# Optimization experiments

Measured on AMD Instinct MI355X. Metric: run time of the kernel, lower is better.

Reference implementation:

```python
import math
import jax, jax.numpy as jnp
import numpy as np

H = 4  # num heads
D = 512
MLP = 1024
EPS = 1e-6


def _ln(x, g, b):
    m = x.mean(-1, keepdims=True)
    v = ((x - m) ** 2).mean(-1, keepdims=True)
    return (x - m) / jnp.sqrt(v + EPS) * g + b


def _heads(x):
    B, S, d = x.shape
    return x.reshape(B, S, H, d // H).transpose(0, 2, 1, 3)  # [B,H,S,hd]


def _att(q, k, v, Wo, bo):
    # q,k,v: [B,S,D] already projected
    hd = q.shape[-1] // H
    qh, kh, vh = _heads(q), _heads(k), _heads(v)
    scores = jnp.einsum('bhqd,bhkd->bhqk', qh, kh) / math.sqrt(hd)
    probs = jax.nn.softmax(scores, axis=-1)
    ctx = jnp.einsum('bhqk,bhkd->bhqd', probs, vh)
    B, _, S, _ = ctx.shape
    ctx = ctx.transpose(0, 2, 1, 3).reshape(B, S, H * hd)
    return ctx @ Wo + bo


def setup_inputs() -> dict:
    key = jax.random.key(0)
    ks = jax.random.split(key, 32)
    i = iter(range(32))
    def w(shape, scale=0.02):
        return jax.random.normal(ks[next(i)], shape, dtype=jnp.float32) * scale
    inp = {
        'x1': jax.random.normal(ks[next(i)], (16, 1024, D), dtype=jnp.float32),
        'x2': jax.random.normal(ks[next(i)], (16, 1024, D), dtype=jnp.float32),
        'ln1_g': jnp.ones((D,), jnp.float32), 'ln1_b': jnp.zeros((D,), jnp.float32),
        'ln2_g': jnp.ones((D,), jnp.float32), 'ln2_b': jnp.zeros((D,), jnp.float32),
        'lnf_g': jnp.ones((D,), jnp.float32), 'lnf_b': jnp.zeros((D,), jnp.float32),
    }
    for name in ['q1', 'k1', 'v1', 'q2', 'k2', 'v2', 'q12', 'k12', 'v12', 'o']:
        inp['W' + name] = w((D, D))
        inp['b' + name] = jnp.zeros((D,), jnp.float32)
    inp['W1'] = w((D, MLP)); inp['b1'] = jnp.zeros((MLP,), jnp.float32)
    inp['W2'] = w((MLP, D)); inp['b2'] = jnp.zeros((D,), jnp.float32)
    return inp


def reference(x1, x2, ln1_g, ln1_b, ln2_g, ln2_b, lnf_g, lnf_b,
              Wq1, bq1, Wk1, bk1, Wv1, bv1,
              Wq2, bq2, Wk2, bk2, Wv2, bv2,
              Wq12, bq12, Wk12, bk12, Wv12, bv12,
              Wo, bo, W1, b1, W2, b2):
    identity = x1
    x1n = _ln(x1, ln1_g, ln1_b)
    x2n = _ln(x2, ln2_g, ln2_b)
    # stream-1 self-attention with residual onto normalized input
    src1 = x1n + _att(x1n @ Wq1 + bq1, x1n @ Wk1 + bk1, x1n @ Wv1 + bv1, Wo, bo)
    # stream-2 self-attention
    src2 = x2n + _att(x2n @ Wq2 + bq2, x2n @ Wk2 + bk2, x2n @ Wv2 + bv2, Wo, bo)
    # cross attention: query from src1, key/value from src2
    attn_out = _att(src1 @ Wq12 + bq12, src2 @ Wk12 + bk12, src2 @ Wv12 + bv12, Wo, bo)
    x = attn_out + identity
    h = _ln(x, lnf_g, lnf_b)
    h = jax.nn.gelu(h @ W1 + b1, approximate=False) @ W2 + b2
    return x + h
```

## Files before the change

kernel.cpp:

```cpp
#include <hip/hip_runtime.h>
#include <math.h>


#define SEQ   1024
#define DM    512
#define HDIM  128
#define MTOK  16384
#define MLPD  1024
#define SC2   ((float)(0.08838834764831845 * 1.4426950408889634))

typedef short bf16x8 __attribute__((ext_vector_type(8)));
typedef float f32x4  __attribute__((ext_vector_type(4)));
typedef float f32x16 __attribute__((ext_vector_type(16)));
typedef unsigned short us4 __attribute__((ext_vector_type(4)));

typedef unsigned int u32g __attribute__((address_space(1)));
typedef unsigned int u32l __attribute__((address_space(3)));

static __device__ __forceinline__ unsigned short f2b(float f) {
  union { float f; unsigned u; } v; v.f = f;
  unsigned r = v.u + 0x7FFFu + ((v.u >> 16) & 1u);
  return (unsigned short)(r >> 16);
}
static __device__ __forceinline__ float b2f(unsigned short h) {
  union { unsigned u; float f; } v; v.u = ((unsigned)h) << 16;
  return v.f;
}
static __device__ __forceinline__ unsigned pk2t(float a, float b) {
  union { float f; unsigned u; } va, vb; va.f = a; vb.f = b;
  return __builtin_amdgcn_perm(vb.u, va.u, 0x07060302u);
}
static __device__ __forceinline__ float ex2(float x) {
  float r; asm("v_exp_f32 %0, %1" : "=v"(r) : "v"(x)); return r;
}
static __device__ __forceinline__ void gl_lds16(const void* g, void* l) {
  __builtin_amdgcn_global_load_lds((u32g*)g, (u32l*)l, 16, 0, 0);
}

struct P12 { const float* p[12]; };
struct P9  { const float* p[9]; };

__global__ __launch_bounds__(256) void prep_kernel(P12 ws, P9 bs,
                                                   unsigned short* __restrict__ WT0,
                                                   unsigned short* __restrict__ W1t,
                                                   unsigned short* __restrict__ W2t,
                                                   float* __restrict__ bcc) {
  int bid = blockIdx.x;
  if (bid >= 3584) {
    int i = (bid - 3584) * 256 + threadIdx.x;
    if (i < 4608) bcc[i] = bs.p[i >> 9][i & 511];
    return;
  }
  __shared__ float t[32][33];
  const float* W; unsigned short* Wt; int K, N, tt;
  if (bid < 2560)      { int wi = bid >> 8; W = ws.p[wi]; Wt = WT0 + (size_t)wi * 262144; K = 512; N = 512; tt = bid & 255; }
  else if (bid < 3072) { W = ws.p[10]; Wt = W1t; K = 512;  N = 1024; tt = bid - 2560; }
  else                 { W = ws.p[11]; Wt = W2t; K = 1024; N = 512;  tt = bid - 3072; }
  int ntiles = N >> 5;
  int bx = tt % ntiles, by = tt / ntiles;
  int n0 = bx * 32, k0 = by * 32;
  int tx = threadIdx.x & 31, ty = threadIdx.x >> 5;
#pragma unroll
  for (int i = 0; i < 32; i += 8)
    t[ty + i][tx] = W[(size_t)(k0 + ty + i) * N + n0 + tx];
  __syncthreads();
#pragma unroll
  for (int i = 0; i < 32; i += 8)
    Wt[(size_t)(n0 + ty + i) * K + k0 + tx] = f2b(t[tx][ty + i]);
}

__global__ __launch_bounds__(256) void ln_kernel(const float* __restrict__ X0,
                                                 const float* __restrict__ X1,
                                                 const float* __restrict__ g0w,
                                                 const float* __restrict__ b0w,
                                                 const float* __restrict__ g1w,
                                                 const float* __restrict__ b1w,
                                                 unsigned short* __restrict__ out0,
                                                 unsigned short* __restrict__ out1) {
  int idx  = blockIdx.x * 4 + (threadIdx.x >> 6);
  int sel  = idx >> 14;
  int row  = idx & 16383;
  const float* X = sel ? X1 : X0;
  const float* gw = sel ? g1w : g0w;
  const float* bw = sel ? b1w : b0w;
  unsigned short* outB = sel ? out1 : out0;
  int lane = threadIdx.x & 63;
  const float4* xr = (const float4*)(X + (size_t)row * DM);
  float4 a = xr[lane];
  float4 c = xr[lane + 64];
  float s  = a.x + a.y + a.z + a.w + c.x + c.y + c.z + c.w;
  float s2 = a.x*a.x + a.y*a.y + a.z*a.z + a.w*a.w
           + c.x*c.x + c.y*c.y + c.z*c.z + c.w*c.w;
#pragma unroll
  for (int off = 1; off < 64; off <<= 1) {
    s  += __shfl_xor(s,  off, 64);
    s2 += __shfl_xor(s2, off, 64);
  }
  float mean = s * (1.0f / 512.0f);
  float var  = s2 * (1.0f / 512.0f) - mean * mean;
  float rstd = rsqrtf(var + 1e-6f);
  const float4* gv = (const float4*)gw;
  const float4* bv = (const float4*)bw;
  float4 g1 = gv[lane], g2 = gv[lane + 64];
  float4 b1 = bv[lane], b2 = bv[lane + 64];
  us4 o1, o2;
  o1.x = f2b((a.x - mean) * rstd * g1.x + b1.x);
  o1.y = f2b((a.y - mean) * rstd * g1.y + b1.y);
  o1.z = f2b((a.z - mean) * rstd * g1.z + b1.z);
  o1.w = f2b((a.w - mean) * rstd * g1.w + b1.w);
  o2.x = f2b((c.x - mean) * rstd * g2.x + b2.x);
  o2.y = f2b((c.y - mean) * rstd * g2.y + b2.y);
  o2.z = f2b((c.z - mean) * rstd * g2.z + b2.z);
  o2.w = f2b((c.w - mean) * rstd * g2.w + b2.w);
  *(us4*)(outB + (size_t)row * DM + lane * 4)        = o1;
  *(us4*)(outB + (size_t)row * DM + (lane + 64) * 4) = o2;
}

template <int RES, bool GELU_ACT, int OMODE>
__global__ __launch_bounds__(256, 2) void gemm_kernel(const unsigned short* __restrict__ A,
                                                      const unsigned short* __restrict__ A1,
                                                      const unsigned short* __restrict__ Bt,
                                                      const float* __restrict__ bias,
                                                      const void* __restrict__ res,
                                                      float* __restrict__ outF,
                                                      unsigned short* __restrict__ outB,
                                                      unsigned short* __restrict__ outV,
                                                      int M, int N, int K) {
  int nT = N >> 7;
  int mT = M >> 7;
  int xcd = blockIdx.x & 7;
  int idx = blockIdx.x >> 3;
  int mPerX = mT >> 3;
  int q = idx / nT;
  int tm = xcd * mPerX + q;
  int tn = idx - q * nT;
  int m0 = tm << 7, n0 = tn << 7;
  int tid = threadIdx.x, lane = tid & 63, w = tid >> 6;
  int m16 = lane & 15, q4 = lane >> 4;
  int wr = (w & 1) << 6, wc = (w >> 1) << 6;
  __shared__ unsigned short Alds[2][128 * 64];
  __shared__ unsigned short Blds[2][128 * 64];
  f32x4 acc[4][4] = {};

  const unsigned short* Aeff = A;
  const unsigned short* Bteff = Bt;
  const float* biaseff = bias;
  if (OMODE == 3) {
    int half = tm >> 7;
    Bteff = Bt + (size_t)half * 3 * 262144;
    biaseff = bias + half * 1536;
  }
  if (OMODE == 4) {
    if (tn >= 4) Aeff = A1;
  }

  int srow = lane >> 3;
  int scol = ((lane & 7) ^ srow) << 3;
  const unsigned short* Ag = Aeff  + (size_t)(m0 + w * 8 + srow) * K + scol;
  const unsigned short* Bg = Bteff + (size_t)(n0 + w * 8 + srow) * K + scol;
  int ldst = w * 512;

#pragma unroll
  for (int it = 0; it < 4; ++it) {
    gl_lds16(Ag + (size_t)it * 32 * K, Alds[0] + it * 2048 + ldst);
    gl_lds16(Bg + (size_t)it * 32 * K, Blds[0] + it * 2048 + ldst);
  }

  int nk = K >> 6;
  for (int ks = 0; ks < nk; ++ks) {
    int cur = ks & 1, nxt = cur ^ 1;
    __syncthreads();
    if (ks + 1 < nk) {
      int k0n = (ks + 1) << 6;
#pragma unroll
      for (int it = 0; it < 4; ++it) {
        gl_lds16(Ag + (size_t)it * 32 * K + k0n, Alds[nxt] + it * 2048 + ldst);
        gl_lds16(Bg + (size_t)it * 32 * K + k0n, Blds[nxt] + it * 2048 + ldst);
      }
    }
    const unsigned short* Ar = Alds[cur];
    const unsigned short* Br = Blds[cur];
#pragma unroll
    for (int kk = 0; kk < 64; kk += 32) {
      bf16x8 af[4], bfr[4];
#pragma unroll
      for (int i = 0; i < 4; ++i) {
        int row = wr + i * 16 + m16;
        af[i] = *(const bf16x8*)(Ar + row * 64 + ((((kk >> 3) + q4) ^ (m16 & 7)) << 3));
      }
#pragma unroll
      for (int j = 0; j < 4; ++j) {
        int row = wc + j * 16 + m16;
        bfr[j] = *(const bf16x8*)(Br + row * 64 + ((((kk >> 3) + q4) ^ (m16 & 7)) << 3));
      }
#pragma unroll
      for (int i = 0; i < 4; ++i)
#pragma unroll
        for (int j = 0; j < 4; ++j)
          acc[i][j] = __builtin_amdgcn_mfma_f32_16x16x32_bf16(af[i], bfr[j], acc[i][j], 0, 0, 0);
    }
  }
  if (OMODE == 3 || OMODE == 4) {
    if (n0 < 1024) {
      int stride = (OMODE == 3) ? 1024 : 512;
      unsigned short* ob = outB;
      int coff = 0;
      if (OMODE == 4 && n0 >= 512) { ob = outB + (size_t)MTOK * 512; coff = 512; }
      float sc = (n0 < 512) ? SC2 : 1.0f;
#pragma unroll
      for (int i = 0; i < 4; ++i) {
#pragma unroll
        for (int r = 0; r < 4; ++r) {
          int row = m0 + wr + i * 16 + q4 * 4 + r;
#pragma unroll
          for (int j = 0; j < 4; ++j) {
            int col = n0 + wc + j * 16 + m16;
            ob[(size_t)row * stride + col - coff] = f2b((acc[i][j][r] + biaseff[col]) * sc);
          }
        }
      }
    } else {
#pragma unroll
      for (int i = 0; i < 4; ++i) {
        int row0 = m0 + wr + i * 16 + q4 * 4;
        int s = row0 & 1023, bl = row0 >> 10;
        s = (s & ~12) | ((s & 4) << 1) | ((s & 8) >> 1);
#pragma unroll
        for (int j = 0; j < 4; ++j) {
          int col = n0 + wc + j * 16 + m16;
          int hh = (col - 1024) >> 7, hd = col & 127;
          float bb = biaseff[col];
          us4 pkv;
          pkv.x = f2b(acc[i][j][0] + bb);
          pkv.y = f2b(acc[i][j][1] + bb);
          pkv.z = f2b(acc[i][j][2] + bb);
          pkv.w = f2b(acc[i][j][3] + bb);
          *(us4*)(outV + (((size_t)(bl * 4 + hh)) * HDIM + hd) * SEQ + s) = pkv;
        }
      }
    }
  } else {
#pragma unroll
    for (int i = 0; i < 4; ++i) {
#pragma unroll
      for (int r = 0; r < 4; ++r) {
        int row = m0 + wr + i * 16 + q4 * 4 + r;
#pragma unroll
        for (int j = 0; j < 4; ++j) {
          int col = n0 + wc + j * 16 + m16;
          float v = acc[i][j][r] + bias[col];
          if (RES == 1) v += ((const float*)res)[(size_t)row * N + col];
          if (RES == 2) v += b2f(((const unsigned short*)res)[(size_t)row * N + col]);
          if (GELU_ACT) v = 0.5f * v * (1.0f + erff(v * 0.70710678118654752f));
          if (OMODE == 1) outF[(size_t)row * N + col] = v;
          else            outB[(size_t)row * N + col] = f2b(v);
        }
      }
    }
  }
}

__global__ __launch_bounds__(256, 2) void attn_kernel(const unsigned short* __restrict__ Qb_,
                                                      const unsigned short* __restrict__ Kb_,
                                                      int tstride,
                                                      const unsigned short* __restrict__ Vt,
                                                      unsigned short* __restrict__ CTX,
                                                      int pairs_per_xcd) {
  int xcd = blockIdx.x & 7;
  int i   = blockIdx.x >> 3;
  int pair = xcd * pairs_per_xcd + (i >> 3);
  int qt   = i & 7;
  int b = pair >> 2, h = pair & 3;
  int tid = threadIdx.x, lane = tid & 63, w = tid >> 6;
  int m32 = lane & 31, hf = lane >> 5;
  size_t qkoff = ((size_t)b * SEQ) * tstride + h * HDIM;
  const unsigned short* Qg = Qb_ + qkoff;
  const unsigned short* Kg = Kb_ + qkoff;
  const unsigned short* Vp = Vt + (size_t)pair * HDIM * SEQ;

  __shared__ unsigned short Klds[2][64 * 128];
  __shared__ unsigned short Vlds[2][128 * 64];

  int qrow0 = qt * 128 + w * 32;
  bf16x8 qf[8];
  {
    const unsigned short* qp = Qg + (size_t)(qrow0 + m32) * tstride + hf * 8;
#pragma unroll
    for (int ks = 0; ks < 8; ++ks) qf[ks] = *(const bf16x8*)(qp + ks * 16);
  }
  bf16x8 onesf;
#pragma unroll
  for (int j = 0; j < 8; ++j) onesf[j] = (short)0x3F80;

  const unsigned short* kp0 = Kg + (size_t)(16 * w + (lane >> 4)) * tstride
                              + (((lane & 15) ^ (lane >> 4)) << 3);
  const unsigned short* kp1 = Kg + (size_t)(16 * w + 4 + (lane >> 4)) * tstride
                              + (((lane & 15) ^ ((lane >> 4) + 4)) << 3);
  const unsigned short* vp0 = Vp + (size_t)(32 * w + (lane >> 3)) * SEQ
                              + (((lane & 7) ^ (lane >> 3)) << 3);
  int klo = 16 * w * 128;
  int vlo = 32 * w * 64;

  gl_lds16(kp0,               Klds[0] + klo);
  gl_lds16(kp1,               Klds[0] + klo + 4 * 128);
  gl_lds16(kp0 + 8 * tstride, Klds[0] + klo + 8 * 128);
  gl_lds16(kp1 + 8 * tstride, Klds[0] + klo + 12 * 128);
  gl_lds16(vp0,               Vlds[0] + vlo);
  gl_lds16(vp0 + 8 * SEQ,     Vlds[0] + vlo + 8 * 64);
  gl_lds16(vp0 + 16 * SEQ,    Vlds[0] + vlo + 16 * 64);
  gl_lds16(vp0 + 24 * SEQ,    Vlds[0] + vlo + 24 * 64);

  f32x16 o0 = {}, o1 = {}, o2 = {}, o3 = {};
  f32x16 lacc = {};

  for (int kt = 0; kt < 16; ++kt) {
    int cur = kt & 1, nxt = cur ^ 1;
    __syncthreads();
    if (kt < 15) {
      kp0 += 64 * tstride; kp1 += 64 * tstride; vp0 += 64;
      gl_lds16(kp0,               Klds[nxt] + klo);
      gl_lds16(kp1,               Klds[nxt] + klo + 4 * 128);
      gl_lds16(kp0 + 8 * tstride, Klds[nxt] + klo + 8 * 128);
      gl_lds16(kp1 + 8 * tstride, Klds[nxt] + klo + 12 * 128);
      gl_lds16(vp0,               Vlds[nxt] + vlo);
      gl_lds16(vp0 + 8 * SEQ,     Vlds[nxt] + vlo + 8 * 64);
      gl_lds16(vp0 + 16 * SEQ,    Vlds[nxt] + vlo + 16 * 64);
      gl_lds16(vp0 + 24 * SEQ,    Vlds[nxt] + vlo + 24 * 64);
    }
    const unsigned short* Kr = Klds[cur];
    const unsigned short* Vr = Vlds[cur];

    f32x16 sc0 = {}, sc1 = {};
#pragma unroll
    for (int ks = 0; ks < 8; ++ks) {
      int ch = 2 * ks + hf;
      bf16x8 kf0 = *(const bf16x8*)(Kr + m32 * 128 + ((ch ^ (m32 & 7)) << 3));
      sc0 = __builtin_amdgcn_mfma_f32_32x32x16_bf16(kf0, qf[ks], sc0, 0, 0, 0);
      int k1r = 32 + m32;
      bf16x8 kf1 = *(const bf16x8*)(Kr + k1r * 128 + ((ch ^ (k1r & 7)) << 3));
      sc1 = __builtin_amdgcn_mfma_f32_32x32x16_bf16(kf1, qf[ks], sc1, 0, 0, 0);
    }

    bf16x8 pa[4];
#pragma unroll
    for (int t = 0; t < 2; ++t) {
      const f32x16& sc = t ? sc1 : sc0;
#pragma unroll
      for (int g = 0; g < 2; ++g) {
        union { unsigned u[4]; bf16x8 v; } uu;
        uu.u[0] = pk2t(ex2(sc[8*g+0]), ex2(sc[8*g+1]));
        uu.u[1] = pk2t(ex2(sc[8*g+2]), ex2(sc[8*g+3]));
        uu.u[2] = pk2t(ex2(sc[8*g+4]), ex2(sc[8*g+5]));
        uu.u[3] = pk2t(ex2(sc[8*g+6]), ex2(sc[8*g+7]));
        pa[2*t + g] = uu.v;
      }
    }

#pragma unroll
    for (int ks = 0; ks < 4; ++ks) {
      int ch = 2 * ks + hf;
      int sw = m32 & 7;
      lacc = __builtin_amdgcn_mfma_f32_32x32x16_bf16(pa[ks], onesf, lacc, 0, 0, 0);
      {
        bf16x8 vf = *(const bf16x8*)(Vr + m32 * 64 + ((ch ^ sw) << 3));
        o0 = __builtin_amdgcn_mfma_f32_32x32x16_bf16(pa[ks], vf, o0, 0, 0, 0);
      }
      {
        bf16x8 vf = *(const bf16x8*)(Vr + (32 + m32) * 64 + ((ch ^ sw) << 3));
        o1 = __builtin_amdgcn_mfma_f32_32x32x16_bf16(pa[ks], vf, o1, 0, 0, 0);
      }
      {
        bf16x8 vf = *(const bf16x8*)(Vr + (64 + m32) * 64 + ((ch ^ sw) << 3));
        o2 = __builtin_amdgcn_mfma_f32_32x32x16_bf16(pa[ks], vf, o2, 0, 0, 0);
      }
      {
        bf16x8 vf = *(const bf16x8*)(Vr + (96 + m32) * 64 + ((ch ^ sw) << 3));
        o3 = __builtin_amdgcn_mfma_f32_32x32x16_bf16(pa[ks], vf, o3, 0, 0, 0);
      }
    }
  }

  size_t obase = ((size_t)b * SEQ + qrow0) * DM + h * HDIM;
#pragma unroll
  for (int g = 0; g < 4; ++g) {
#pragma unroll
    for (int r = 0; r < 4; ++r) {
      int reg = 4 * g + r;
      int rowl = 8 * g + 4 * hf + r;
      float inv = 1.0f / lacc[reg];
      size_t off = obase + (size_t)rowl * DM + m32;
      CTX[off]      = f2b(o0[reg] * inv);
      CTX[off + 32] = f2b(o1[reg] * inv);
      CTX[off + 64] = f2b(o2[reg] * inv);
      CTX[off + 96] = f2b(o3[reg] * inv);
    }
  }
}

extern "C" void kernel_launch(void* const* d_in, const int* in_sizes, int n_in,
                              void* d_out, int out_size, void* d_ws, size_t ws_size,
                              hipStream_t stream) {
  const float* x1    = (const float*)d_in[0];
  const float* x2    = (const float*)d_in[1];
  const float* ln1_g = (const float*)d_in[2];
  const float* ln1_b = (const float*)d_in[3];
  const float* ln2_g = (const float*)d_in[4];
  const float* ln2_b = (const float*)d_in[5];
  const float* lnf_g = (const float*)d_in[6];
  const float* lnf_b = (const float*)d_in[7];
  P12 wsrc;
  for (int i = 0; i < 10; ++i) wsrc.p[i] = (const float*)d_in[8 + 2 * i];
  wsrc.p[10] = (const float*)d_in[28];
  wsrc.p[11] = (const float*)d_in[30];
  P9 bsrc;
  for (int i = 0; i < 9; ++i) bsrc.p[i] = (const float*)d_in[9 + 2 * i];
  const float* bo   = (const float*)d_in[27];
  const float* b1   = (const float*)d_in[29];
  const float* b2   = (const float*)d_in[31];

  char* ws = (char*)d_ws;
  size_t off = 0;
  auto alloc = [&](size_t bytes) -> char* {
    char* p = ws + off;
    off += (bytes + 255) & ~(size_t)255;
    return p;
  };
  unsigned short* WT0 = (unsigned short*)alloc((size_t)10 * 512 * 512 * 2);
  auto WT = [&](int i) { return WT0 + (size_t)i * 262144; };
  unsigned short* W1t = (unsigned short*)alloc((size_t)1024 * 512 * 2);
  unsigned short* W2t = (unsigned short*)alloc((size_t)512 * 1024 * 2);
  float*          bcc = (float*)alloc(4608 * 4);
  unsigned short* XN  = (unsigned short*)alloc((size_t)2 * MTOK * DM * 2);
  unsigned short* QKb = (unsigned short*)alloc((size_t)2 * MTOK * 1024 * 2);
  unsigned short* Vtb = (unsigned short*)alloc((size_t)128 * HDIM * SEQ * 2);
  unsigned short* CT  = (unsigned short*)alloc((size_t)2 * MTOK * DM * 2);
  float*          Xf  = (float*)alloc((size_t)MTOK * DM * 4);
  unsigned short* XN1 = XN + (size_t)MTOK * DM;
  unsigned short* MID = QKb;
  unsigned short* HN  = Vtb;
  float* bias_self  = bcc;
  float* bias_cross = bcc + 3072;

  prep_kernel<<<3602, 256, 0, stream>>>(wsrc, bsrc, WT0, W1t, W2t, bcc);

  ln_kernel<<<2 * MTOK / 4, 256, 0, stream>>>(x1, x2, ln1_g, ln1_b, ln2_g, ln2_b, XN, XN1);

  gemm_kernel<0, false, 3><<<3072, 256, 0, stream>>>(XN, nullptr, WT0, bias_self,
      nullptr, nullptr, QKb, Vtb, 32768, 1536, 512);

  attn_kernel<<<128 * 8, 256, 0, stream>>>(QKb, QKb + 512, 1024, Vtb, CT, 16);

  gemm_kernel<2, false, 0><<<1024, 256, 0, stream>>>(CT, nullptr, WT(9), bo, XN,
      nullptr, XN, nullptr, 32768, 512, 512);

  gemm_kernel<0, false, 4><<<1536, 256, 0, stream>>>(XN, XN1, WT(6), bias_cross,
      nullptr, nullptr, QKb, Vtb, 16384, 1536, 512);

  attn_kernel<<<64 * 8, 256, 0, stream>>>(QKb, QKb + (size_t)MTOK * 512, 512, Vtb, CT, 8);

  gemm_kernel<1, false, 1><<<512, 256, 0, stream>>>(CT, nullptr, WT(9), bo, x1,
      Xf, nullptr, nullptr, 16384, 512, 512);

  ln_kernel<<<MTOK / 4, 256, 0, stream>>>(Xf, Xf, lnf_g, lnf_b, lnf_g, lnf_b, HN, HN);

  gemm_kernel<0, true,  0><<<1024, 256, 0, stream>>>(HN, nullptr, W1t, b1,
      nullptr, nullptr, MID, nullptr, 16384, 1024, 512);
  gemm_kernel<1, false, 1><<<512, 256, 0, stream>>>(MID, nullptr, W2t, b2,
      Xf, (float*)d_out, nullptr, nullptr, 16384, 512, 1024);
}
```

Before: 515.1 us.

## Software-pipeline attention loop so QK of next tile overlaps PV of current

Restructures the flash-attention inner loop into a software pipeline: the QK^T MFMAs for tile t+1 are issued alongside the PV MFMAs for tile t, with the exp/pack step deferred. The goal is to hide the exp2/packing latency and the LDS reads behind independent matrix work. The cost is an extra barrier per iteration, because the buffer being restaged must be fully consumed first, and more live registers for the second set of probability fragments, which could lower occupancy.

```diff
diff --git a/kernel.cpp b/kernel.cpp
--- a/kernel.cpp
+++ b/kernel.cpp
@@ -301,84 +301,103 @@
   int klo = 16 * w * 128;
   int vlo = 32 * w * 64;
 
-  gl_lds16(kp0,               Klds[0] + klo);
-  gl_lds16(kp1,               Klds[0] + klo + 4 * 128);
-  gl_lds16(kp0 + 8 * tstride, Klds[0] + klo + 8 * 128);
-  gl_lds16(kp1 + 8 * tstride, Klds[0] + klo + 12 * 128);
-  gl_lds16(vp0,               Vlds[0] + vlo);
-  gl_lds16(vp0 + 8 * SEQ,     Vlds[0] + vlo + 8 * 64);
-  gl_lds16(vp0 + 16 * SEQ,    Vlds[0] + vlo + 16 * 64);
-  gl_lds16(vp0 + 24 * SEQ,    Vlds[0] + vlo + 24 * 64);
+  auto stage = [&](unsigned short* Kb, unsigned short* Vb) {
+    gl_lds16(kp0,               Kb + klo);
+    gl_lds16(kp1,               Kb + klo + 4 * 128);
+    gl_lds16(kp0 + 8 * tstride, Kb + klo + 8 * 128);
+    gl_lds16(kp1 + 8 * tstride, Kb + klo + 12 * 128);
+    gl_lds16(vp0,               Vb + vlo);
+    gl_lds16(vp0 + 8 * SEQ,     Vb + vlo + 8 * 64);
+    gl_lds16(vp0 + 16 * SEQ,    Vb + vlo + 16 * 64);
+    gl_lds16(vp0 + 24 * SEQ,    Vb + vlo + 24 * 64);
+  };
+  auto adv = [&]() { kp0 += 64 * tstride; kp1 += 64 * tstride; vp0 += 64; };
 
   f32x16 o0 = {}, o1 = {}, o2 = {}, o3 = {};
   f32x16 lacc = {};
-
-  for (int kt = 0; kt < 16; ++kt) {
-    int cur = kt & 1, nxt = cur ^ 1;
-    __syncthreads();
-    if (kt < 15) {
-      kp0 += 64 * tstride; kp1 += 64 * tstride; vp0 += 64;
-      gl_lds16(kp0,               Klds[nxt] + klo);
-      gl_lds16(kp1,               Klds[nxt] + klo + 4 * 128);
-      gl_lds16(kp0 + 8 * tstride, Klds[nxt] + klo + 8 * 128);
-      gl_lds16(kp1 + 8 * tstride, Klds[nxt] + klo + 12 * 128);
-      gl_lds16(vp0,               Vlds[nxt] + vlo);
-      gl_lds16(vp0 + 8 * SEQ,     Vlds[nxt] + vlo + 8 * 64);
-      gl_lds16(vp0 + 16 * SEQ,    Vlds[nxt] + vlo + 16 * 64);
-      gl_lds16(vp0 + 24 * SEQ,    Vlds[nxt] + vlo + 24 * 64);
-    }
-    const unsigned short* Kr = Klds[cur];
-    const unsigned short* Vr = Vlds[cur];
-
-    f32x16 sc0 = {}, sc1 = {};
+  bf16x8 pa0, pa1, pa2, pa3;
+  bf16x8 pb0, pb1, pb2, pb3;
+
+  auto qk = [&](const unsigned short* Kr, f32x16& s0, f32x16& s1) {
 #pragma unroll
     for (int ks = 0; ks < 8; ++ks) {
       int ch = 2 * ks + hf;
       bf16x8 kf0 = *(const bf16x8*)(Kr + m32 * 128 + ((ch ^ (m32 & 7)) << 3));
-      sc0 = __builtin_amdgcn_mfma_f32_32x32x16_bf16(kf0, qf[ks], sc0, 0, 0, 0);
+      s0 = __builtin_amdgcn_mfma_f32_32x32x16_bf16(kf0, qf[ks], s0, 0, 0, 0);
       int k1r = 32 + m32;
       bf16x8 kf1 = *(const bf16x8*)(Kr + k1r * 128 + ((ch ^ (k1r & 7)) << 3));
-      sc1 = __builtin_amdgcn_mfma_f32_32x32x16_bf16(kf1, qf[ks], sc1, 0, 0, 0);
-    }
-
-    bf16x8 pa[4];
-#pragma unroll
-    for (int t = 0; t < 2; ++t) {
-      const f32x16& sc = t ? sc1 : sc0;
-#pragma unroll
-      for (int g = 0; g < 2; ++g) {
-        union { unsigned u[4]; bf16x8 v; } uu;
-        uu.u[0] = pk2t(ex2(sc[8*g+0]), ex2(sc[8*g+1]));
-        uu.u[1] = pk2t(ex2(sc[8*g+2]), ex2(sc[8*g+3]));
-        uu.u[2] = pk2t(ex2(sc[8*g+4]), ex2(sc[8*g+5]));
-        uu.u[3] = pk2t(ex2(sc[8*g+6]), ex2(sc[8*g+7]));
-        pa[2*t + g] = uu.v;
-      }
-    }
-
+      s1 = __builtin_amdgcn_mfma_f32_32x32x16_bf16(kf1, qf[ks], s1, 0, 0, 0);
+    }
+  };
+  auto mkpa = [&](const f32x16& s0, const f32x16& s1,
+                  bf16x8& q0, bf16x8& q1, bf16x8& q2, bf16x8& q3) {
+    union { unsigned u[4]; bf16x8 v; } uu;
+#pragma unroll
+    for (int g = 0; g < 2; ++g) {
+      uu.u[0] = pk2t(ex2(s0[8*g+0]), ex2(s0[8*g+1]));
+      uu.u[1] = pk2t(ex2(s0[8*g+2]), ex2(s0[8*g+3]));
+      uu.u[2] = pk2t(ex2(s0[8*g+4]), ex2(s0[8*g+5]));
+      uu.u[3] = pk2t(ex2(s0[8*g+6]), ex2(s0[8*g+7]));
+      if (g == 0) q0 = uu.v; else q1 = uu.v;
+    }
+#pragma unroll
+    for (int g = 0; g < 2; ++g) {
+      uu.u[0] = pk2t(ex2(s1[8*g+0]), ex2(s1[8*g+1]));
+      uu.u[1] = pk2t(ex2(s1[8*g+2]), ex2(s1[8*g+3]));
+      uu.u[2] = pk2t(ex2(s1[8*g+4]), ex2(s1[8*g+5]));
+      uu.u[3] = pk2t(ex2(s1[8*g+6]), ex2(s1[8*g+7]));
+      if (g == 0) q2 = uu.v; else q3 = uu.v;
+    }
+  };
+  auto pv = [&](const unsigned short* Vr,
+                const bf16x8& q0, const bf16x8& q1, const bf16x8& q2, const bf16x8& q3) {
 #pragma unroll
     for (int ks = 0; ks < 4; ++ks) {
+      const bf16x8& pk = (ks == 0) ? q0 : (ks == 1) ? q1 : (ks == 2) ? q2 : q3;
       int ch = 2 * ks + hf;
       int sw = m32 & 7;
-      lacc = __builtin_amdgcn_mfma_f32_32x32x16_bf16(pa[ks], onesf, lacc, 0, 0, 0);
+      lacc = __builtin_amdgcn_mfma_f32_32x32x16_bf16(pk, onesf, lacc, 0, 0, 0);
       {
         bf16x8 vf = *(const bf16x8*)(Vr + m32 * 64 + ((ch ^ sw) << 3));
-        o0 = __builtin_amdgcn_mfma_f32_32x32x16_bf16(pa[ks], vf, o0, 0, 0, 0);
+        o0 = __builtin_amdgcn_mfma_f32_32x32x16_bf16(pk, vf, o0, 0, 0, 0);
       }
       {
         bf16x8 vf = *(const bf16x8*)(Vr + (32 + m32) * 64 + ((ch ^ sw) << 3));
-        o1 = __builtin_amdgcn_mfma_f32_32x32x16_bf16(pa[ks], vf, o1, 0, 0, 0);
+        o1 = __builtin_amdgcn_mfma_f32_32x32x16_bf16(pk, vf, o1, 0, 0, 0);
       }
       {
         bf16x8 vf = *(const bf16x8*)(Vr + (64 + m32) * 64 + ((ch ^ sw) << 3));
-        o2 = __builtin_amdgcn_mfma_f32_32x32x16_bf16(pa[ks], vf, o2, 0, 0, 0);
+        o2 = __builtin_amdgcn_mfma_f32_32x32x16_bf16(pk, vf, o2, 0, 0, 0);
       }
       {
         bf16x8 vf = *(const bf16x8*)(Vr + (96 + m32) * 64 + ((ch ^ sw) << 3));
-        o3 = __builtin_amdgcn_mfma_f32_32x32x16_bf16(pa[ks], vf, o3, 0, 0, 0);
-      }
-    }
-  }
+        o3 = __builtin_amdgcn_mfma_f32_32x32x16_bf16(pk, vf, o3, 0, 0, 0);
+      }
+    }
+  };
+
+  stage(Klds[0], Vlds[0]);
+  __syncthreads();
+  adv();
+  stage(Klds[1], Vlds[1]);
+  {
+    f32x16 s0 = {}, s1 = {};
+    qk(Klds[0], s0, s1);
+    mkpa(s0, s1, pa0, pa1, pa2, pa3);
+  }
+
+  for (int t = 0; t < 15; ++t) {
+    int cur = t & 1, nxt = cur ^ 1;
+    __syncthreads();
+    f32x16 s0 = {}, s1 = {};
+    qk(Klds[nxt], s0, s1);
+    pv(Vlds[cur], pa0, pa1, pa2, pa3);
+    mkpa(s0, s1, pb0, pb1, pb2, pb3);
+    __syncthreads();
+    if (t < 14) { adv(); stage(Klds[cur], Vlds[cur]); }
+    pa0 = pb0; pa1 = pb1; pa2 = pb2; pa3 = pb3;
+  }
+  pv(Vlds[1], pa0, pa1, pa2, pa3);
 
   size_t obase = ((size_t)b * SEQ + qrow0) * DM + h * HDIM;
 #pragma unroll
```

New measurement: 506.5 us. No clear change (-1.7%).
